# Optimization experiments

Hardware: AMD Instinct MI355X
Metric: run time of the kernel (lower is better)

The kernel has to match this reference:

```python
import jax, jax.numpy as jnp
import numpy as np

STAGE_NUM = 5
BETA = 1.0
EPS = 1e-6


def _em_refine(cls, proto):
    # cls: [b, d]; proto: [k, d]. Matches torch einsum('bd,bkd->bk') with
    # batch-replicated prototypes == cls @ proto.T (no (b,k,d) materialization).
    p = proto
    for _ in range(STAGE_NUM):
        r = jax.nn.softmax(cls @ p.T, axis=1)          # [b, k]
        p = r.T @ cls                                   # [k, d]
        p = p / (jnp.linalg.norm(p, axis=1, keepdims=True) + EPS)
    return p


def setup_inputs() -> dict:
    key = jax.random.key(0)
    k1, k2 = jax.random.split(key)
    b, d, k = 8192, 1024, 512
    cls = jax.random.normal(k1, (b, d), dtype=jnp.float32)
    proto = jax.random.normal(k2, (k, d), dtype=jnp.float32)
    # __init__ normalizes prototypes to unit norm (with 1e-6 in denominator)
    proto = proto / (1e-6 + jnp.linalg.norm(proto, axis=1, keepdims=True))
    return {"cls": cls, "prototypes": proto}


def reference(cls, prototypes):
    # EM loop runs under torch.no_grad() -> stop_gradient here.
    new_proto = jax.lax.stop_gradient(_em_refine(cls, prototypes))  # [k, d]
    dot = cls @ new_proto.T                                          # [b, k]
    r = jax.nn.softmax(dot, axis=1)
    z_recon = r @ new_proto                                          # [b, d]
    z_out = BETA * z_recon + cls
    return (r, z_out)
```

## Files before the change

### kernel.cpp

```cpp
#include <hip/hip_runtime.h>

typedef short v8s __attribute__((ext_vector_type(8)));
typedef _Float16 v8h __attribute__((ext_vector_type(8)));
typedef float v4f __attribute__((ext_vector_type(4)));

typedef __attribute__((address_space(1))) const void* as1_void_cp;
typedef __attribute__((address_space(3))) void* as3_void_p;

__device__ __forceinline__ unsigned short f2bf(float x) {
  union { float f; unsigned int u; } v; v.f = x;
  unsigned int r = v.u + 0x7fffu + ((v.u >> 16) & 1u);
  return (unsigned short)(r >> 16);
}
__device__ __forceinline__ float bf2f(unsigned short h) {
  union { unsigned int u; float f; } v; v.u = ((unsigned int)h) << 16;
  return v.f;
}
__device__ __forceinline__ unsigned short f2h(float x) {
  _Float16 h = (_Float16)x;
  return __builtin_bit_cast(unsigned short, h);
}

struct B3 { int x, y, z; };
__device__ __forceinline__ B3 xcd_swizzle() {
  const int gx = gridDim.x, gy = gridDim.y;
  const int nwg = gx * gy * gridDim.z;
  int flat = blockIdx.x + gx * (blockIdx.y + gy * blockIdx.z);
  if ((nwg & 7) == 0) flat = (flat & 7) * (nwg >> 3) + (flat >> 3);
  B3 b;
  b.x = flat % gx;
  b.y = (flat / gx) % gy;
  b.z = flat / (gx * gy);
  return b;
}

template <bool ADD, bool F16>
__global__ __launch_bounds__(256) void gemm_bt(
    const unsigned short* __restrict__ A, const unsigned short* __restrict__ B,
    float* __restrict__ C, const float* __restrict__ Cadd,
    int N, int lda, int ldb, int klen, size_t csplit) {
  __shared__ __align__(16) unsigned short As[2][128 * 64];
  __shared__ __align__(16) unsigned short Bs[2][128 * 64];
  const int tid = threadIdx.x;
  const B3 bid = xcd_swizzle();
  const int bn = bid.x * 128, bm = bid.y * 128;
  const int k0 = bid.z * klen;
  float* Cp = C + (size_t)bid.z * csplit;

  const unsigned short* ag0 = A + (size_t)(bm + (tid >> 2)) * lda + ((tid & 3) << 3) + k0;
  const unsigned short* ag1 = ag0 + (size_t)64 * lda;
  const unsigned short* bg0 = B + (size_t)(bn + (tid >> 2)) * ldb + ((tid & 3) << 3) + k0;
  const unsigned short* bg1 = bg0 + (size_t)64 * ldb;

  const int lane = tid & 63;
  const int q = lane >> 4, m15 = lane & 15;
  const int w = tid >> 6;
  const int wr = (w >> 1) * 64, wc = (w & 1) * 64;

  v4f acc[4][4];
#pragma unroll
  for (int i = 0; i < 4; ++i)
#pragma unroll
    for (int j = 0; j < 4; ++j) acc[i][j] = 0.f;

  auto stage = [&](int kk, int b) {
    unsigned short* al = As[b] + tid * 8;
    unsigned short* bl = Bs[b] + tid * 8;
    __builtin_amdgcn_global_load_lds((as1_void_cp)(ag0 + kk), (as3_void_p)al, 16, 0, 0);
    __builtin_amdgcn_global_load_lds((as1_void_cp)(ag1 + kk), (as3_void_p)(al + 2048), 16, 0, 0);
    __builtin_amdgcn_global_load_lds((as1_void_cp)(ag0 + kk + 32), (as3_void_p)(al + 4096), 16, 0, 0);
    __builtin_amdgcn_global_load_lds((as1_void_cp)(ag1 + kk + 32), (as3_void_p)(al + 6144), 16, 0, 0);
    __builtin_amdgcn_global_load_lds((as1_void_cp)(bg0 + kk), (as3_void_p)bl, 16, 0, 0);
    __builtin_amdgcn_global_load_lds((as1_void_cp)(bg1 + kk), (as3_void_p)(bl + 2048), 16, 0, 0);
    __builtin_amdgcn_global_load_lds((as1_void_cp)(bg0 + kk + 32), (as3_void_p)(bl + 4096), 16, 0, 0);
    __builtin_amdgcn_global_load_lds((as1_void_cp)(bg1 + kk + 32), (as3_void_p)(bl + 6144), 16, 0, 0);
  };

  const int nt = klen >> 6;
  stage(0, 0);
  if (nt > 1) stage(64, 1);
  for (int t = 0; t < nt; ++t) {
    if (t + 1 < nt)
      asm volatile("s_waitcnt vmcnt(8)" ::: "memory");
    else
      asm volatile("s_waitcnt vmcnt(0)" ::: "memory");
    __builtin_amdgcn_s_barrier();
    const unsigned short* Ab = As[t & 1];
    const unsigned short* Bb = Bs[t & 1];
#pragma unroll
    for (int h = 0; h < 2; ++h) {
      v8s af[4], bf[4];
#pragma unroll
      for (int i = 0; i < 4; ++i)
        af[i] = *(const v8s*)(Ab + h * 4096 + (wr + i * 16 + m15) * 32 + q * 8);
#pragma unroll
      for (int j = 0; j < 4; ++j)
        bf[j] = *(const v8s*)(Bb + h * 4096 + (wc + j * 16 + m15) * 32 + q * 8);
#pragma unroll
      for (int i = 0; i < 4; ++i)
#pragma unroll
        for (int j = 0; j < 4; ++j) {
          if constexpr (F16)
            acc[i][j] = __builtin_amdgcn_mfma_f32_16x16x32_f16(
                __builtin_bit_cast(v8h, af[i]), __builtin_bit_cast(v8h, bf[j]), acc[i][j], 0, 0, 0);
          else
            acc[i][j] = __builtin_amdgcn_mfma_f32_16x16x32_bf16(af[i], bf[j], acc[i][j], 0, 0, 0);
        }
    }
    if (t + 2 < nt) {
      __builtin_amdgcn_s_barrier();
      stage((t + 2) << 6, t & 1);
    }
  }

#pragma unroll
  for (int i = 0; i < 4; ++i) {
#pragma unroll
    for (int j = 0; j < 4; ++j) {
      const int col = bn + wc + j * 16 + m15;
#pragma unroll
      for (int rr = 0; rr < 4; ++rr) {
        const int row = bm + wr + i * 16 + q * 4 + rr;
        const size_t idx = (size_t)row * N + col;
        float v = acc[i][j][rr];
        if (ADD) v += Cadd[idx];
        Cp[idx] = v;
      }
    }
  }
}

__global__ __launch_bounds__(256) void gemm_bt64(
    const unsigned short* __restrict__ A, const unsigned short* __restrict__ B,
    float* __restrict__ C, int N, int lda, int ldb, int klen, size_t csplit) {
  __shared__ __align__(16) unsigned short As[2][64 * 64];
  __shared__ __align__(16) unsigned short Bs[2][128 * 64];
  const int tid = threadIdx.x;
  const B3 bid = xcd_swizzle();
  const int bn = bid.x * 128, bm = bid.y * 64;
  const int k0 = bid.z * klen;
  float* Cp = C + (size_t)bid.z * csplit;

  const unsigned short* ag0 = A + (size_t)(bm + (tid >> 2)) * lda + ((tid & 3) << 3) + k0;
  const unsigned short* bg0 = B + (size_t)(bn + (tid >> 2)) * ldb + ((tid & 3) << 3) + k0;
  const unsigned short* bg1 = bg0 + (size_t)64 * ldb;

  const int lane = tid & 63;
  const int q = lane >> 4, m15 = lane & 15;
  const int w = tid >> 6;
  const int wr = (w >> 1) * 32, wc = (w & 1) * 64;

  v4f acc[2][4];
#pragma unroll
  for (int i = 0; i < 2; ++i)
#pragma unroll
    for (int j = 0; j < 4; ++j) acc[i][j] = 0.f;

  auto stage = [&](int kk, int b) {
    unsigned short* al = As[b] + tid * 8;
    unsigned short* bl = Bs[b] + tid * 8;
    __builtin_amdgcn_global_load_lds((as1_void_cp)(ag0 + kk), (as3_void_p)al, 16, 0, 0);
    __builtin_amdgcn_global_load_lds((as1_void_cp)(ag0 + kk + 32), (as3_void_p)(al + 2048), 16, 0, 0);
    __builtin_amdgcn_global_load_lds((as1_void_cp)(bg0 + kk), (as3_void_p)bl, 16, 0, 0);
    __builtin_amdgcn_global_load_lds((as1_void_cp)(bg1 + kk), (as3_void_p)(bl + 2048), 16, 0, 0);
    __builtin_amdgcn_global_load_lds((as1_void_cp)(bg0 + kk + 32), (as3_void_p)(bl + 4096), 16, 0, 0);
    __builtin_amdgcn_global_load_lds((as1_void_cp)(bg1 + kk + 32), (as3_void_p)(bl + 6144), 16, 0, 0);
  };

  const int nt = klen >> 6;
  stage(0, 0);
  if (nt > 1) stage(64, 1);
  for (int t = 0; t < nt; ++t) {
    if (t + 1 < nt)
      asm volatile("s_waitcnt vmcnt(6)" ::: "memory");
    else
      asm volatile("s_waitcnt vmcnt(0)" ::: "memory");
    __builtin_amdgcn_s_barrier();
    const unsigned short* Ab = As[t & 1];
    const unsigned short* Bb = Bs[t & 1];
#pragma unroll
    for (int h = 0; h < 2; ++h) {
      v8s af[2], bf[4];
#pragma unroll
      for (int i = 0; i < 2; ++i)
        af[i] = *(const v8s*)(Ab + h * 2048 + (wr + i * 16 + m15) * 32 + q * 8);
#pragma unroll
      for (int j = 0; j < 4; ++j)
        bf[j] = *(const v8s*)(Bb + h * 4096 + (wc + j * 16 + m15) * 32 + q * 8);
#pragma unroll
      for (int i = 0; i < 2; ++i)
#pragma unroll
        for (int j = 0; j < 4; ++j)
          acc[i][j] = __builtin_amdgcn_mfma_f32_16x16x32_f16(
              __builtin_bit_cast(v8h, af[i]), __builtin_bit_cast(v8h, bf[j]), acc[i][j], 0, 0, 0);
    }
    if (t + 2 < nt) {
      __builtin_amdgcn_s_barrier();
      stage((t + 2) << 6, t & 1);
    }
  }

#pragma unroll
  for (int i = 0; i < 2; ++i) {
#pragma unroll
    for (int j = 0; j < 4; ++j) {
      const int col = bn + wc + j * 16 + m15;
#pragma unroll
      for (int rr = 0; rr < 4; ++rr) {
        const int row = bm + wr + i * 16 + q * 4 + rr;
        Cp[(size_t)row * N + col] = acc[i][j][rr];
      }
    }
  }
}

__global__ __launch_bounds__(256) void gemm_bt3(
    const unsigned short* __restrict__ Ah, const unsigned short* __restrict__ Al,
    const unsigned short* __restrict__ Bh, const unsigned short* __restrict__ Bl,
    float* __restrict__ C, int N, int lda, int ldb, int klen, size_t csplit) {
  __shared__ __align__(16) unsigned short Ash[2][128 * 32];
  __shared__ __align__(16) unsigned short Asl[2][128 * 32];
  __shared__ __align__(16) unsigned short Bsh[2][128 * 32];
  __shared__ __align__(16) unsigned short Bsl[2][128 * 32];
  const int tid = threadIdx.x;
  const B3 bid = xcd_swizzle();
  const int bn = bid.x * 128, bm = bid.y * 128;
  const int k0 = bid.z * klen;
  float* Cp = C + (size_t)bid.z * csplit;

  const size_t aoff = (size_t)(bm + (tid >> 2)) * lda + ((tid & 3) << 3) + k0;
  const size_t boff = (size_t)(bn + (tid >> 2)) * ldb + ((tid & 3) << 3) + k0;
  const unsigned short* agh0 = Ah + aoff;
  const unsigned short* agh1 = agh0 + (size_t)64 * lda;
  const unsigned short* agl0 = Al + aoff;
  const unsigned short* agl1 = agl0 + (size_t)64 * lda;
  const unsigned short* bgh0 = Bh + boff;
  const unsigned short* bgh1 = bgh0 + (size_t)64 * ldb;
  const unsigned short* bgl0 = Bl + boff;
  const unsigned short* bgl1 = bgl0 + (size_t)64 * ldb;

  const int lane = tid & 63;
  const int q = lane >> 4, m15 = lane & 15;
  const int w = tid >> 6;
  const int wr = (w >> 1) * 64, wc = (w & 1) * 64;

  v4f acc[4][4];
#pragma unroll
  for (int i = 0; i < 4; ++i)
#pragma unroll
    for (int j = 0; j < 4; ++j) acc[i][j] = 0.f;

  auto stage = [&](int kk, int b) {
    __builtin_amdgcn_global_load_lds((as1_void_cp)(agh0 + kk), (as3_void_p)(Ash[b] + tid * 8), 16, 0, 0);
    __builtin_amdgcn_global_load_lds((as1_void_cp)(agh1 + kk), (as3_void_p)(Ash[b] + 2048 + tid * 8), 16, 0, 0);
    __builtin_amdgcn_global_load_lds((as1_void_cp)(agl0 + kk), (as3_void_p)(Asl[b] + tid * 8), 16, 0, 0);
    __builtin_amdgcn_global_load_lds((as1_void_cp)(agl1 + kk), (as3_void_p)(Asl[b] + 2048 + tid * 8), 16, 0, 0);
    __builtin_amdgcn_global_load_lds((as1_void_cp)(bgh0 + kk), (as3_void_p)(Bsh[b] + tid * 8), 16, 0, 0);
    __builtin_amdgcn_global_load_lds((as1_void_cp)(bgh1 + kk), (as3_void_p)(Bsh[b] + 2048 + tid * 8), 16, 0, 0);
    __builtin_amdgcn_global_load_lds((as1_void_cp)(bgl0 + kk), (as3_void_p)(Bsl[b] + tid * 8), 16, 0, 0);
    __builtin_amdgcn_global_load_lds((as1_void_cp)(bgl1 + kk), (as3_void_p)(Bsl[b] + 2048 + tid * 8), 16, 0, 0);
  };

  const int nt = klen >> 5;
  stage(0, 0);
  if (nt > 1) stage(32, 1);
  for (int t = 0; t < nt; ++t) {
    if (t + 1 < nt)
      asm volatile("s_waitcnt vmcnt(8)" ::: "memory");
    else
      asm volatile("s_waitcnt vmcnt(0)" ::: "memory");
    __builtin_amdgcn_s_barrier();
    const int b = t & 1;
    v8s afh[4], afl[4], bfh[4], bfl[4];
#pragma unroll
    for (int i = 0; i < 4; ++i) {
      const int ro = (wr + i * 16 + m15) * 32 + q * 8;
      afh[i] = *(const v8s*)(Ash[b] + ro);
      afl[i] = *(const v8s*)(Asl[b] + ro);
    }
#pragma unroll
    for (int j = 0; j < 4; ++j) {
      const int ro = (wc + j * 16 + m15) * 32 + q * 8;
      bfh[j] = *(const v8s*)(Bsh[b] + ro);
      bfl[j] = *(const v8s*)(Bsl[b] + ro);
    }
#pragma unroll
    for (int i = 0; i < 4; ++i)
#pragma unroll
      for (int j = 0; j < 4; ++j) {
        acc[i][j] = __builtin_amdgcn_mfma_f32_16x16x32_bf16(afh[i], bfh[j], acc[i][j], 0, 0, 0);
        acc[i][j] = __builtin_amdgcn_mfma_f32_16x16x32_bf16(afh[i], bfl[j], acc[i][j], 0, 0, 0);
        acc[i][j] = __builtin_amdgcn_mfma_f32_16x16x32_bf16(afl[i], bfh[j], acc[i][j], 0, 0, 0);
      }
    if (t + 2 < nt) {
      __builtin_amdgcn_s_barrier();
      stage((t + 2) << 5, b);
    }
  }

#pragma unroll
  for (int i = 0; i < 4; ++i) {
#pragma unroll
    for (int j = 0; j < 4; ++j) {
      const int col = bn + wc + j * 16 + m15;
#pragma unroll
      for (int rr = 0; rr < 4; ++rr) {
        const int row = bm + wr + i * 16 + q * 4 + rr;
        Cp[(size_t)row * N + col] = acc[i][j][rr];
      }
    }
  }
}

__global__ __launch_bounds__(256) void cast_split_transpose_cls(
    const float* __restrict__ cls,
    unsigned short* __restrict__ ch, unsigned short* __restrict__ cl,
    unsigned short* __restrict__ cTh, unsigned short* __restrict__ cTl,
    unsigned short* __restrict__ cg, unsigned short* __restrict__ cTg) {
  __shared__ unsigned short th[64][72];
  __shared__ unsigned short tl[64][72];
  const int d0 = blockIdx.x * 64, b0 = blockIdx.y * 64;
  const int t = threadIdx.x;
#pragma unroll
  for (int i = 0; i < 4; ++i) {
    int flat = t + i * 256;
    int bl_ = flat >> 4;
    int dl = (flat & 15) << 2;
    float4 v = *(const float4*)(cls + (size_t)(b0 + bl_) * 1024 + d0 + dl);
    ushort4 h, l, g;
    h.x = f2bf(v.x); l.x = f2bf(v.x - bf2f(h.x)); g.x = f2h(bf2f(h.x) + bf2f(l.x));
    h.y = f2bf(v.y); l.y = f2bf(v.y - bf2f(h.y)); g.y = f2h(bf2f(h.y) + bf2f(l.y));
    h.z = f2bf(v.z); l.z = f2bf(v.z - bf2f(h.z)); g.z = f2h(bf2f(h.z) + bf2f(l.z));
    h.w = f2bf(v.w); l.w = f2bf(v.w - bf2f(h.w)); g.w = f2h(bf2f(h.w) + bf2f(l.w));
    *(ushort4*)(ch + (size_t)(b0 + bl_) * 1024 + d0 + dl) = h;
    *(ushort4*)(cl + (size_t)(b0 + bl_) * 1024 + d0 + dl) = l;
    *(ushort4*)(cg + (size_t)(b0 + bl_) * 1024 + d0 + dl) = g;
    th[bl_][dl] = h.x; th[bl_][dl + 1] = h.y; th[bl_][dl + 2] = h.z; th[bl_][dl + 3] = h.w;
    tl[bl_][dl] = l.x; tl[bl_][dl + 1] = l.y; tl[bl_][dl + 2] = l.z; tl[bl_][dl + 3] = l.w;
  }
  __syncthreads();
#pragma unroll
  for (int i = 0; i < 4; ++i) {
    int flat = t + i * 256;
    int dl = flat >> 4;
    int bl_ = (flat & 15) << 2;
    ushort4 h = make_ushort4(th[bl_][dl], th[bl_ + 1][dl], th[bl_ + 2][dl], th[bl_ + 3][dl]);
    ushort4 l = make_ushort4(tl[bl_][dl], tl[bl_ + 1][dl], tl[bl_ + 2][dl], tl[bl_ + 3][dl]);
    ushort4 g;
    g.x = f2h(bf2f(h.x) + bf2f(l.x));
    g.y = f2h(bf2f(h.y) + bf2f(l.y));
    g.z = f2h(bf2f(h.z) + bf2f(l.z));
    g.w = f2h(bf2f(h.w) + bf2f(l.w));
    *(ushort4*)(cTh + (size_t)(d0 + dl) * 8192 + b0 + bl_) = h;
    *(ushort4*)(cTl + (size_t)(d0 + dl) * 8192 + b0 + bl_) = l;
    *(ushort4*)(cTg + (size_t)(d0 + dl) * 8192 + b0 + bl_) = g;
  }
}

__global__ __launch_bounds__(256) void split_f32(const float* __restrict__ in,
                                                 unsigned short* __restrict__ hi,
                                                 unsigned short* __restrict__ lo) {
  const size_t i = (size_t)(blockIdx.x * blockDim.x + threadIdx.x) * 4;
  float4 v = *(const float4*)(in + i);
  ushort4 h, l;
  h.x = f2bf(v.x); l.x = f2bf(v.x - bf2f(h.x));
  h.y = f2bf(v.y); l.y = f2bf(v.y - bf2f(h.y));
  h.z = f2bf(v.z); l.z = f2bf(v.z - bf2f(h.z));
  h.w = f2bf(v.w); l.w = f2bf(v.w - bf2f(h.w));
  *(ushort4*)(hi + i) = h;
  *(ushort4*)(lo + i) = l;
}

template <bool HILO, bool SPLIT>
__global__ __launch_bounds__(512) void rowsoftmax_T(
    const float* __restrict__ SP0, const float* __restrict__ SP1,
    unsigned short* __restrict__ rTh, unsigned short* __restrict__ rTl) {
  __shared__ __align__(16) unsigned short th[32 * 520];
  __shared__ __align__(16) unsigned short tl[HILO ? 32 * 520 : 8];
  const int t = threadIdx.x;
  const int lane = t & 63, w = t >> 6;
  const int b0 = blockIdx.x * 32;
#pragma unroll
  for (int k = 0; k < 4; ++k) {
    const int bl = w * 4 + k;
    const int row = b0 + bl;
    const size_t off = (size_t)row * 512 + lane * 8;
    float4 v0 = *(const float4*)(SP0 + off);
    float4 v1 = *(const float4*)(SP0 + off + 4);
    float e[8];
    e[0] = v0.x; e[1] = v0.y; e[2] = v0.z; e[3] = v0.w;
    e[4] = v1.x; e[5] = v1.y; e[6] = v1.z; e[7] = v1.w;
    if constexpr (SPLIT) {
      float4 u0 = *(const float4*)(SP1 + off);
      float4 u1 = *(const float4*)(SP1 + off + 4);
      e[0] += u0.x; e[1] += u0.y; e[2] += u0.z; e[3] += u0.w;
      e[4] += u1.x; e[5] += u1.y; e[6] += u1.z; e[7] += u1.w;
    }
    float m = fmaxf(fmaxf(fmaxf(e[0], e[1]), fmaxf(e[2], e[3])),
                    fmaxf(fmaxf(e[4], e[5]), fmaxf(e[6], e[7])));
    for (int o = 32; o; o >>= 1) m = fmaxf(m, __shfl_xor(m, o));
    float s = 0.f;
#pragma unroll
    for (int i = 0; i < 8; ++i) { e[i] = __expf(e[i] - m); s += e[i]; }
    for (int o = 32; o; o >>= 1) s += __shfl_xor(s, o);
    const float inv = 1.f / s;
    unsigned short ph[8], pl[8];
#pragma unroll
    for (int i = 0; i < 8; ++i) {
      const float r = e[i] * inv;
      if constexpr (HILO) {
        ph[i] = f2bf(r);
        pl[i] = f2bf(r - bf2f(ph[i]));
      } else {
        ph[i] = f2h(r);
      }
    }
    *(v8s*)&th[bl * 520 + lane * 8] = *(v8s*)ph;
    if constexpr (HILO) *(v8s*)&tl[bl * 520 + lane * 8] = *(v8s*)pl;
  }
  __syncthreads();
  const int c = t;
  unsigned short uh[32];
#pragma unroll
  for (int b = 0; b < 32; ++b) uh[b] = th[b * 520 + c];
#pragma unroll
  for (int q = 0; q < 4; ++q)
    *(v8s*)(rTh + (size_t)c * 8192 + b0 + q * 8) = *(v8s*)&uh[q * 8];
  if constexpr (HILO) {
    unsigned short ul[32];
#pragma unroll
    for (int b = 0; b < 32; ++b) ul[b] = tl[b * 520 + c];
#pragma unroll
    for (int q = 0; q < 4; ++q)
      *(v8s*)(rTl + (size_t)c * 8192 + b0 + q * 8) = *(v8s*)&ul[q * 8];
  }
}

__global__ __launch_bounds__(256) void softmax_rows(const float* __restrict__ SP0,
                                                    float* __restrict__ r_out,
                                                    unsigned short* __restrict__ r_g) {
  const int w = threadIdx.x >> 6, lane = threadIdx.x & 63;
  const int row = blockIdx.x * 4 + w;
  const size_t off = (size_t)row * 512 + lane * 8;
  float4 v0 = *(const float4*)(SP0 + off);
  float4 v1 = *(const float4*)(SP0 + off + 4);
  float m = fmaxf(fmaxf(fmaxf(v0.x, v0.y), fmaxf(v0.z, v0.w)),
                  fmaxf(fmaxf(v1.x, v1.y), fmaxf(v1.z, v1.w)));
  for (int off2 = 32; off2; off2 >>= 1) m = fmaxf(m, __shfl_xor(m, off2));
  float e0 = __expf(v0.x - m), e1 = __expf(v0.y - m), e2 = __expf(v0.z - m), e3 = __expf(v0.w - m);
  float e4 = __expf(v1.x - m), e5 = __expf(v1.y - m), e6 = __expf(v1.z - m), e7 = __expf(v1.w - m);
  float s = e0 + e1 + e2 + e3 + e4 + e5 + e6 + e7;
  for (int off2 = 32; off2; off2 >>= 1) s += __shfl_xor(s, off2);
  const float inv = 1.f / s;
  e0 *= inv; e1 *= inv; e2 *= inv; e3 *= inv; e4 *= inv; e5 *= inv; e6 *= inv; e7 *= inv;
  float* rp = r_out + off;
  *(float4*)rp = make_float4(e0, e1, e2, e3);
  *(float4*)(rp + 4) = make_float4(e4, e5, e6, e7);
  unsigned short* bp = r_g + off;
  *(ushort4*)bp = make_ushort4(f2h(e0), f2h(e1), f2h(e2), f2h(e3));
  *(ushort4*)(bp + 4) = make_ushort4(f2h(e4), f2h(e5), f2h(e6), f2h(e7));
}

template <int NS>
__global__ __launch_bounds__(256) void reduce_normalize(const float* __restrict__ Pp,
                                                        unsigned short* __restrict__ pg,
                                                        unsigned short* __restrict__ pTg) {
  __shared__ float red[4];
  const int c = blockIdx.x, t = threadIdx.x;
  float ax = 0.f, ay = 0.f, az = 0.f, aw = 0.f;
#pragma unroll
  for (int s = 0; s < NS; ++s) {
    const float4 v = *(const float4*)(Pp + ((size_t)s * 512 + c) * 1024 + t * 4);
    ax += v.x; ay += v.y; az += v.z; aw += v.w;
  }
  float ss = ax * ax + ay * ay + az * az + aw * aw;
  for (int off = 32; off; off >>= 1) ss += __shfl_xor(ss, off);
  const int w = t >> 6, lane = t & 63;
  if (!lane) red[w] = ss;
  __syncthreads();
  const float tot = red[0] + red[1] + red[2] + red[3];
  const float scale = 1.f / (sqrtf(tot) + 1e-6f);
  ax *= scale; ay *= scale; az *= scale; aw *= scale;
  *(ushort4*)(pg + (size_t)c * 1024 + t * 4) =
      make_ushort4(f2h(ax), f2h(ay), f2h(az), f2h(aw));
  pTg[(size_t)(t * 4 + 0) * 512 + c] = f2h(ax);
  pTg[(size_t)(t * 4 + 1) * 512 + c] = f2h(ay);
  pTg[(size_t)(t * 4 + 2) * 512 + c] = f2h(az);
  pTg[(size_t)(t * 4 + 3) * 512 + c] = f2h(aw);
}

extern "C" void kernel_launch(void* const* d_in, const int* in_sizes, int n_in,
                              void* d_out, int out_size, void* d_ws, size_t ws_size,
                              hipStream_t stream) {
  const float* cls = (const float*)d_in[0];
  const float* proto = (const float*)d_in[1];
  float* out_r = (float*)d_out;
  float* out_z = out_r + (size_t)8192 * 512;

  char* w = (char*)d_ws;
  unsigned short* cls_h = (unsigned short*)w; w += (size_t)8192 * 1024 * 2;
  unsigned short* cls_l = (unsigned short*)w; w += (size_t)8192 * 1024 * 2;
  unsigned short* clsT_h = (unsigned short*)w; w += (size_t)1024 * 8192 * 2;
  unsigned short* clsT_l = (unsigned short*)w; w += (size_t)1024 * 8192 * 2;
  unsigned short* cls_g = (unsigned short*)w; w += (size_t)8192 * 1024 * 2;
  unsigned short* clsT_g = (unsigned short*)w; w += (size_t)1024 * 8192 * 2;
  unsigned short* p_h = (unsigned short*)w; w += (size_t)512 * 1024 * 2;
  unsigned short* p_l = (unsigned short*)w; w += (size_t)512 * 1024 * 2;
  unsigned short* p_g = (unsigned short*)w; w += (size_t)512 * 1024 * 2;
  unsigned short* pT_g = (unsigned short*)w; w += (size_t)1024 * 512 * 2;
  unsigned short* rT_h = (unsigned short*)w; w += (size_t)512 * 8192 * 2;
  unsigned short* rT_l = (unsigned short*)w; w += (size_t)512 * 8192 * 2;
  float* SP = (float*)w;
  float* SP1 = SP + (size_t)8192 * 512;

  cast_split_transpose_cls<<<dim3(16, 128), 256, 0, stream>>>(
      cls, cls_h, cls_l, clsT_h, clsT_l, cls_g, clsT_g);
  split_f32<<<512, 256, 0, stream>>>(proto, p_h, p_l);

  gemm_bt3<<<dim3(4, 64, 2), 256, 0, stream>>>(cls_h, cls_l, p_h, p_l, SP,
                                               512, 1024, 1024, 512,
                                               (size_t)8192 * 512);
  rowsoftmax_T<true, true><<<256, 512, 0, stream>>>(SP, SP1, rT_h, rT_l);
  gemm_bt3<<<dim3(8, 4, 16), 256, 0, stream>>>(rT_h, rT_l, clsT_h, clsT_l, SP,
                                               1024, 8192, 8192, 512,
                                               (size_t)512 * 1024);
  reduce_normalize<16><<<512, 256, 0, stream>>>(SP, p_g, pT_g);

  for (int it = 0; it < 4; ++it) {
    gemm_bt64<<<dim3(4, 128, 1), 256, 0, stream>>>(cls_g, p_g, SP,
                                                   512, 1024, 1024, 1024, 0);
    rowsoftmax_T<false, false><<<256, 512, 0, stream>>>(SP, nullptr, rT_h, nullptr);
    gemm_bt64<<<dim3(8, 8, 8), 256, 0, stream>>>(rT_h, clsT_g, SP,
                                                 1024, 8192, 8192, 1024,
                                                 (size_t)512 * 1024);
    reduce_normalize<8><<<512, 256, 0, stream>>>(SP, p_g, pT_g);
  }

  gemm_bt64<<<dim3(4, 128, 1), 256, 0, stream>>>(cls_g, p_g, SP,
                                                 512, 1024, 1024, 1024, 0);
  softmax_rows<<<2048, 256, 0, stream>>>(SP, out_r, rT_h);
  gemm_bt<true, true><<<dim3(8, 64, 1), 256, 0, stream>>>(rT_h, pT_g, out_z, cls,
                                                          1024, 512, 512, 512, 0);
}
```

Before: 436.9 us.

## Triple-buffer gemm_bt64 and add non-split-K 64-row bf16x3 GEMM for first stage

Extends the f16 64-row GEMM from double to triple buffering, so two tiles of global-to-LDS loads are in flight while one is computed, with a wait ladder on vmcnt. Adds a new 64x128-tile bf16x3 (hi/lo split) GEMM with the same three-stage pipeline and uses it for the first logits GEMM instead of the split-K 128-tile kernel. This removes the second partial buffer and the reduction of split-K partials inside the first softmax. The cost is more LDS per block, which may reduce occupancy.

```diff
diff --git a/kernel.cpp b/kernel.cpp
--- a/kernel.cpp
+++ b/kernel.cpp
@@ -33,6 +33,14 @@
   b.z = flat / (gx * gy);
   return b;
 }
+
+#define WAIT_LADDER(rem, W2, W1)                              \
+  if ((rem) >= 2)                                             \
+    asm volatile("s_waitcnt vmcnt(" #W2 ")" ::: "memory");    \
+  else if ((rem) == 1)                                        \
+    asm volatile("s_waitcnt vmcnt(" #W1 ")" ::: "memory");    \
+  else                                                        \
+    asm volatile("s_waitcnt vmcnt(0)" ::: "memory")
 
 template <bool ADD, bool F16>
 __global__ __launch_bounds__(256) void gemm_bt(
@@ -133,8 +141,8 @@
 __global__ __launch_bounds__(256) void gemm_bt64(
     const unsigned short* __restrict__ A, const unsigned short* __restrict__ B,
     float* __restrict__ C, int N, int lda, int ldb, int klen, size_t csplit) {
-  __shared__ __align__(16) unsigned short As[2][64 * 64];
-  __shared__ __align__(16) unsigned short Bs[2][128 * 64];
+  __shared__ __align__(16) unsigned short As[3][64 * 64];
+  __shared__ __align__(16) unsigned short Bs[3][128 * 64];
   const int tid = threadIdx.x;
   const B3 bid = xcd_swizzle();
   const int bn = bid.x * 128, bm = bid.y * 64;
@@ -170,14 +178,14 @@
   const int nt = klen >> 6;
   stage(0, 0);
   if (nt > 1) stage(64, 1);
+  if (nt > 2) stage(128, 2);
   for (int t = 0; t < nt; ++t) {
-    if (t + 1 < nt)
-      asm volatile("s_waitcnt vmcnt(6)" ::: "memory");
-    else
-      asm volatile("s_waitcnt vmcnt(0)" ::: "memory");
+    const int rem = nt - 1 - t;
+    WAIT_LADDER(rem, 12, 6);
     __builtin_amdgcn_s_barrier();
-    const unsigned short* Ab = As[t & 1];
-    const unsigned short* Bb = Bs[t & 1];
+    const int b = t % 3;
+    const unsigned short* Ab = As[b];
+    const unsigned short* Bb = Bs[b];
 #pragma unroll
     for (int h = 0; h < 2; ++h) {
       v8s af[2], bf[4];
@@ -194,9 +202,9 @@
           acc[i][j] = __builtin_amdgcn_mfma_f32_16x16x32_f16(
               __builtin_bit_cast(v8h, af[i]), __builtin_bit_cast(v8h, bf[j]), acc[i][j], 0, 0, 0);
     }
-    if (t + 2 < nt) {
+    if (t + 3 < nt) {
       __builtin_amdgcn_s_barrier();
-      stage((t + 2) << 6, t & 1);
+      stage((t + 3) << 6, b);
     }
   }
 
@@ -209,6 +217,95 @@
       for (int rr = 0; rr < 4; ++rr) {
         const int row = bm + wr + i * 16 + q * 4 + rr;
         Cp[(size_t)row * N + col] = acc[i][j][rr];
+      }
+    }
+  }
+}
+
+__global__ __launch_bounds__(256) void gemm_bt3_64(
+    const unsigned short* __restrict__ Ah, const unsigned short* __restrict__ Al,
+    const unsigned short* __restrict__ Bh, const unsigned short* __restrict__ Bl,
+    float* __restrict__ C, int N, int lda, int ldb, int klen) {
+  __shared__ __align__(16) unsigned short Ash[3][64 * 32];
+  __shared__ __align__(16) unsigned short Asl[3][64 * 32];
+  __shared__ __align__(16) unsigned short Bsh[3][128 * 32];
+  __shared__ __align__(16) unsigned short Bsl[3][128 * 32];
+  const int tid = threadIdx.x;
+  const B3 bid = xcd_swizzle();
+  const int bn = bid.x * 128, bm = bid.y * 64;
+
+  const unsigned short* agh = Ah + (size_t)(bm + (tid >> 2)) * lda + ((tid & 3) << 3);
+  const unsigned short* agl = Al + (size_t)(bm + (tid >> 2)) * lda + ((tid & 3) << 3);
+  const unsigned short* bgh0 = Bh + (size_t)(bn + (tid >> 2)) * ldb + ((tid & 3) << 3);
+  const unsigned short* bgh1 = bgh0 + (size_t)64 * ldb;
+  const unsigned short* bgl0 = Bl + (size_t)(bn + (tid >> 2)) * ldb + ((tid & 3) << 3);
+  const unsigned short* bgl1 = bgl0 + (size_t)64 * ldb;
+
+  const int lane = tid & 63;
+  const int q = lane >> 4, m15 = lane & 15;
+  const int w = tid >> 6;
+  const int wr = (w >> 1) * 32, wc = (w & 1) * 64;
+
+  v4f acc[2][4];
+#pragma unroll
+  for (int i = 0; i < 2; ++i)
+#pragma unroll
+    for (int j = 0; j < 4; ++j) acc[i][j] = 0.f;
+
+  auto stage = [&](int kk, int b) {
+    __builtin_amdgcn_global_load_lds((as1_void_cp)(agh + kk), (as3_void_p)(Ash[b] + tid * 8), 16, 0, 0);
+    __builtin_amdgcn_global_load_lds((as1_void_cp)(agl + kk), (as3_void_p)(Asl[b] + tid * 8), 16, 0, 0);
+    __builtin_amdgcn_global_load_lds((as1_void_cp)(bgh0 + kk), (as3_void_p)(Bsh[b] + tid * 8), 16, 0, 0);
+    __builtin_amdgcn_global_load_lds((as1_void_cp)(bgh1 + kk), (as3_void_p)(Bsh[b] + 2048 + tid * 8), 16, 0, 0);
+    __builtin_amdgcn_global_load_lds((as1_void_cp)(bgl0 + kk), (as3_void_p)(Bsl[b] + tid * 8), 16, 0, 0);
+    __builtin_amdgcn_global_load_lds((as1_void_cp)(bgl1 + kk), (as3_void_p)(Bsl[b] + 2048 + tid * 8), 16, 0, 0);
+  };
+
+  const int nt = klen >> 5;
+  stage(0, 0);
+  if (nt > 1) stage(32, 1);
+  if (nt > 2) stage(64, 2);
+  for (int t = 0; t < nt; ++t) {
+    const int rem = nt - 1 - t;
+    WAIT_LADDER(rem, 12, 6);
+    __builtin_amdgcn_s_barrier();
+    const int b = t % 3;
+    v8s afh[2], afl[2], bfh[4], bfl[4];
+#pragma unroll
+    for (int i = 0; i < 2; ++i) {
+      const int ro = (wr + i * 16 + m15) * 32 + q * 8;
+      afh[i] = *(const v8s*)(Ash[b] + ro);
+      afl[i] = *(const v8s*)(Asl[b] + ro);
+    }
+#pragma unroll
+    for (int j = 0; j < 4; ++j) {
+      const int ro = (wc + j * 16 + m15) * 32 + q * 8;
+      bfh[j] = *(const v8s*)(Bsh[b] + ro);
+      bfl[j] = *(const v8s*)(Bsl[b] + ro);
+    }
+#pragma unroll
+    for (int i = 0; i < 2; ++i)
+#pragma unroll
+      for (int j = 0; j < 4; ++j) {
+        acc[i][j] = __builtin_amdgcn_mfma_f32_16x16x32_bf16(afh[i], bfh[j], acc[i][j], 0, 0, 0);
+        acc[i][j] = __builtin_amdgcn_mfma_f32_16x16x32_bf16(afh[i], bfl[j], acc[i][j], 0, 0, 0);
+        acc[i][j] = __builtin_amdgcn_mfma_f32_16x16x32_bf16(afl[i], bfh[j], acc[i][j], 0, 0, 0);
+      }
+    if (t + 3 < nt) {
+      __builtin_amdgcn_s_barrier();
+      stage((t + 3) << 5, b);
+    }
+  }
+
+#pragma unroll
+  for (int i = 0; i < 2; ++i) {
+#pragma unroll
+    for (int j = 0; j < 4; ++j) {
+      const int col = bn + wc + j * 16 + m15;
+#pragma unroll
+      for (int rr = 0; rr < 4; ++rr) {
+        const int row = bm + wr + i * 16 + q * 4 + rr;
+        C[(size_t)row * N + col] = acc[i][j][rr];
       }
     }
   }
@@ -517,10 +614,9 @@
       cls, cls_h, cls_l, clsT_h, clsT_l, cls_g, clsT_g);
   split_f32<<<512, 256, 0, stream>>>(proto, p_h, p_l);
 
-  gemm_bt3<<<dim3(4, 64, 2), 256, 0, stream>>>(cls_h, cls_l, p_h, p_l, SP,
-                                               512, 1024, 1024, 512,
-                                               (size_t)8192 * 512);
-  rowsoftmax_T<true, true><<<256, 512, 0, stream>>>(SP, SP1, rT_h, rT_l);
+  gemm_bt3_64<<<dim3(4, 128, 1), 256, 0, stream>>>(cls_h, cls_l, p_h, p_l, SP,
+                                                   512, 1024, 1024, 1024);
+  rowsoftmax_T<true, false><<<256, 512, 0, stream>>>(SP, nullptr, rT_h, rT_l);
   gemm_bt3<<<dim3(8, 4, 16), 256, 0, stream>>>(rT_h, rT_l, clsT_h, clsT_l, SP,
                                                1024, 8192, 8192, 512,
                                                (size_t)512 * 1024);
```

After: 447.0 us. 1.02x slower.

## XOR-swizzle LDS tile layout in all GEMMs and triple-buffer gemm_bt64

Applied to the files above, without the earlier changes.

Each thread's global source column is permuted with an XOR of its row bits, so data lands in LDS in a swizzled order. The fragment reads apply the matching XOR to undo it, which is meant to reduce LDS bank conflicts on the 16-byte MFMA operand loads. Separately, gemm_bt64 moves from double to triple buffering with a deeper vmcnt wait ladder, keeping two tiles in flight to hide global latency. The cost is more LDS per block in gemm_bt64, which may lower occupancy.

```diff
diff --git a/kernel.cpp b/kernel.cpp
--- a/kernel.cpp
+++ b/kernel.cpp
@@ -33,6 +33,16 @@
   b.z = flat / (gx * gy);
   return b;
 }
+
+#define WAIT_LADDER(rem, W2, W1)                              \
+  if ((rem) >= 2)                                             \
+    asm volatile("s_waitcnt vmcnt(" #W2 ")" ::: "memory");    \
+  else if ((rem) == 1)                                        \
+    asm volatile("s_waitcnt vmcnt(" #W1 ")" ::: "memory");    \
+  else                                                        \
+    asm volatile("s_waitcnt vmcnt(0)" ::: "memory")
+
+#define SRC_COL(tid) ((((tid) & 3) ^ (((tid) >> 3) & 3)) << 3)
 
 template <bool ADD, bool F16>
 __global__ __launch_bounds__(256) void gemm_bt(
@@ -47,13 +57,14 @@
   const int k0 = bid.z * klen;
   float* Cp = C + (size_t)bid.z * csplit;
 
-  const unsigned short* ag0 = A + (size_t)(bm + (tid >> 2)) * lda + ((tid & 3) << 3) + k0;
+  const unsigned short* ag0 = A + (size_t)(bm + (tid >> 2)) * lda + SRC_COL(tid) + k0;
   const unsigned short* ag1 = ag0 + (size_t)64 * lda;
-  const unsigned short* bg0 = B + (size_t)(bn + (tid >> 2)) * ldb + ((tid & 3) << 3) + k0;
+  const unsigned short* bg0 = B + (size_t)(bn + (tid >> 2)) * ldb + SRC_COL(tid) + k0;
   const unsigned short* bg1 = bg0 + (size_t)64 * ldb;
 
   const int lane = tid & 63;
   const int q = lane >> 4, m15 = lane & 15;
+  const int qs = (q ^ ((m15 >> 1) & 3)) * 8;
   const int w = tid >> 6;
   const int wr = (w >> 1) * 64, wc = (w & 1) * 64;
 
@@ -92,10 +103,10 @@
       v8s af[4], bf[4];
 #pragma unroll
       for (int i = 0; i < 4; ++i)
-        af[i] = *(const v8s*)(Ab + h * 4096 + (wr + i * 16 + m15) * 32 + q * 8);
+        af[i] = *(const v8s*)(Ab + h * 4096 + (wr + i * 16 + m15) * 32 + qs);
 #pragma unroll
       for (int j = 0; j < 4; ++j)
-        bf[j] = *(const v8s*)(Bb + h * 4096 + (wc + j * 16 + m15) * 32 + q * 8);
+        bf[j] = *(const v8s*)(Bb + h * 4096 + (wc + j * 16 + m15) * 32 + qs);
 #pragma unroll
       for (int i = 0; i < 4; ++i)
 #pragma unroll
@@ -133,20 +144,21 @@
 __global__ __launch_bounds__(256) void gemm_bt64(
     const unsigned short* __restrict__ A, const unsigned short* __restrict__ B,
     float* __restrict__ C, int N, int lda, int ldb, int klen, size_t csplit) {
-  __shared__ __align__(16) unsigned short As[2][64 * 64];
-  __shared__ __align__(16) unsigned short Bs[2][128 * 64];
+  __shared__ __align__(16) unsigned short As[3][64 * 64];
+  __shared__ __align__(16) unsigned short Bs[3][128 * 64];
   const int tid = threadIdx.x;
   const B3 bid = xcd_swizzle();
   const int bn = bid.x * 128, bm = bid.y * 64;
   const int k0 = bid.z * klen;
   float* Cp = C + (size_t)bid.z * csplit;
 
-  const unsigned short* ag0 = A + (size_t)(bm + (tid >> 2)) * lda + ((tid & 3) << 3) + k0;
-  const unsigned short* bg0 = B + (size_t)(bn + (tid >> 2)) * ldb + ((tid & 3) << 3) + k0;
+  const unsigned short* ag0 = A + (size_t)(bm + (tid >> 2)) * lda + SRC_COL(tid) + k0;
+  const unsigned short* bg0 = B + (size_t)(bn + (tid >> 2)) * ldb + SRC_COL(tid) + k0;
   const unsigned short* bg1 = bg0 + (size_t)64 * ldb;
 
   const int lane = tid & 63;
   const int q = lane >> 4, m15 = lane & 15;
+  const int qs = (q ^ ((m15 >> 1) & 3)) * 8;
   const int w = tid >> 6;
   const int wr = (w >> 1) * 32, wc = (w & 1) * 64;
 
@@ -170,23 +182,23 @@
   const int nt = klen >> 6;
   stage(0, 0);
   if (nt > 1) stage(64, 1);
+  if (nt > 2) stage(128, 2);
   for (int t = 0; t < nt; ++t) {
-    if (t + 1 < nt)
-      asm volatile("s_waitcnt vmcnt(6)" ::: "memory");
-    else
-      asm volatile("s_waitcnt vmcnt(0)" ::: "memory");
+    const int rem = nt - 1 - t;
+    WAIT_LADDER(rem, 12, 6);
     __builtin_amdgcn_s_barrier();
-    const unsigned short* Ab = As[t & 1];
-    const unsigned short* Bb = Bs[t & 1];
+    const int b = t % 3;
+    const unsigned short* Ab = As[b];
+    const unsigned short* Bb = Bs[b];
 #pragma unroll
     for (int h = 0; h < 2; ++h) {
       v8s af[2], bf[4];
 #pragma unroll
       for (int i = 0; i < 2; ++i)
-        af[i] = *(const v8s*)(Ab + h * 2048 + (wr + i * 16 + m15) * 32 + q * 8);
+        af[i] = *(const v8s*)(Ab + h * 2048 + (wr + i * 16 + m15) * 32 + qs);
 #pragma unroll
       for (int j = 0; j < 4; ++j)
-        bf[j] = *(const v8s*)(Bb + h * 4096 + (wc + j * 16 + m15) * 32 + q * 8);
+        bf[j] = *(const v8s*)(Bb + h * 4096 + (wc + j * 16 + m15) * 32 + qs);
 #pragma unroll
       for (int i = 0; i < 2; ++i)
 #pragma unroll
@@ -194,9 +206,9 @@
           acc[i][j] = __builtin_amdgcn_mfma_f32_16x16x32_f16(
               __builtin_bit_cast(v8h, af[i]), __builtin_bit_cast(v8h, bf[j]), acc[i][j], 0, 0, 0);
     }
-    if (t + 2 < nt) {
+    if (t + 3 < nt) {
       __builtin_amdgcn_s_barrier();
-      stage((t + 2) << 6, t & 1);
+      stage((t + 3) << 6, b);
     }
   }
 
@@ -228,8 +240,8 @@
   const int k0 = bid.z * klen;
   float* Cp = C + (size_t)bid.z * csplit;
 
-  const size_t aoff = (size_t)(bm + (tid >> 2)) * lda + ((tid & 3) << 3) + k0;
-  const size_t boff = (size_t)(bn + (tid >> 2)) * ldb + ((tid & 3) << 3) + k0;
+  const size_t aoff = (size_t)(bm + (tid >> 2)) * lda + SRC_COL(tid) + k0;
+  const size_t boff = (size_t)(bn + (tid >> 2)) * ldb + SRC_COL(tid) + k0;
   const unsigned short* agh0 = Ah + aoff;
   const unsigned short* agh1 = agh0 + (size_t)64 * lda;
   const unsigned short* agl0 = Al + aoff;
@@ -241,6 +253,7 @@
 
   const int lane = tid & 63;
   const int q = lane >> 4, m15 = lane & 15;
+  const int qs = (q ^ ((m15 >> 1) & 3)) * 8;
   const int w = tid >> 6;
   const int wr = (w >> 1) * 64, wc = (w & 1) * 64;
 
@@ -274,13 +287,13 @@
     v8s afh[4], afl[4], bfh[4], bfl[4];
 #pragma unroll
     for (int i = 0; i < 4; ++i) {
-      const int ro = (wr + i * 16 + m15) * 32 + q * 8;
+      const int ro = (wr + i * 16 + m15) * 32 + qs;
       afh[i] = *(const v8s*)(Ash[b] + ro);
       afl[i] = *(const v8s*)(Asl[b] + ro);
     }
 #pragma unroll
     for (int j = 0; j < 4; ++j) {
-      const int ro = (wc + j * 16 + m15) * 32 + q * 8;
+      const int ro = (wc + j * 16 + m15) * 32 + qs;
       bfh[j] = *(const v8s*)(Bsh[b] + ro);
       bfl[j] = *(const v8s*)(Bsl[b] + ro);
     }
```

New measurement: 441.6 us. Within noise of the previous version (+1.1%).
